# Performance work log

Measured on AMD Instinct MI355X. Metric: run time of the kernel, lower is better.

The kernel has to match this reference:

```python
import jax, jax.numpy as jnp
import numpy as np

N, S, D_MODEL, H = 8, 1024, 1024, 16
D = D_MODEL // H
NEG = -1e9


def setup_inputs() -> dict:
    key = jax.random.key(0)
    ks = jax.random.split(key, 12)
    s = 0.02
    q = jax.random.normal(ks[0], (N, S, D_MODEL), jnp.float32)
    k = jax.random.normal(ks[1], (N, S, D_MODEL), jnp.float32)
    v = jax.random.normal(ks[2], (N, S, D_MODEL), jnp.float32)
    # causal mask: 1 where masked (strict upper triangle)
    causal_mask = jnp.triu(jnp.ones((S, S), jnp.int32), k=1)
    # padding mask: 1 where key position is padding
    padding_mask = jax.random.randint(ks[3], (N, S), 0, 2, jnp.int32)
    Wq = jax.random.normal(ks[4], (D_MODEL, D_MODEL), jnp.float32) * s
    bq = jnp.zeros((D_MODEL,), jnp.float32)
    Wk = jax.random.normal(ks[5], (D_MODEL, D_MODEL), jnp.float32) * s
    bk = jnp.zeros((D_MODEL,), jnp.float32)
    Wv = jax.random.normal(ks[6], (D_MODEL, D_MODEL), jnp.float32) * s
    bv = jnp.zeros((D_MODEL,), jnp.float32)
    Wo = jax.random.normal(ks[7], (D_MODEL, D_MODEL), jnp.float32) * s
    bo = jnp.zeros((D_MODEL,), jnp.float32)
    return {"q": q, "k": k, "v": v, "causal_mask": causal_mask,
            "padding_mask": padding_mask, "Wq": Wq, "bq": bq, "Wk": Wk,
            "bk": bk, "Wv": Wv, "bv": bv, "Wo": Wo, "bo": bo}


def reference(q, k, v, causal_mask, padding_mask, Wq, bq, Wk, bk, Wv, bv, Wo, bo):
    n, qs, _ = q.shape
    # projections (nn.Linear: x @ W.T + b)
    qp = (q @ Wq.T + bq).reshape(n, qs, H, D).transpose(0, 2, 1, 3)  # [N,H,qS,D]
    kp = (k @ Wk.T + bk).reshape(n, -1, H, D).transpose(0, 2, 1, 3)  # [N,H,kS,D]
    vp = (v @ Wv.T + bv).reshape(n, -1, H, D).transpose(0, 2, 1, 3)  # [N,H,kS,D]
    # NOTE: faithful to source -- scale by sqrt(d_model), not sqrt(d_head)
    score = jnp.einsum('bhqd,bhkd->bhqk', qp, kp) / jnp.sqrt(jnp.float32(D_MODEL))
    score = jnp.where(causal_mask[None, None, :, :] == 1, NEG, score)
    score = jnp.where(padding_mask[:, None, None, :] == 1, NEG, score)
    w = jax.nn.softmax(score, axis=-1)  # dropout is identity in eval mode
    x = jnp.einsum('bhqk,bhkd->bhqd', w, vp)  # [N,H,qS,D]
    x = x.transpose(0, 2, 1, 3).reshape(n, qs, D_MODEL)
    x = x @ Wo.T + bo
    return (x, w)
```

## Files before the change

kernel.cpp:

```cpp
#include <hip/hip_runtime.h>

typedef __bf16 bf16;
typedef bf16 bf16x8 __attribute__((ext_vector_type(8)));
typedef bf16 bf16x4 __attribute__((ext_vector_type(4)));
typedef float f32x4 __attribute__((ext_vector_type(4)));

#define S_LEN 1024
#define DM    1024
#define NH    16
#define HD    64
#define NB    8
#define NEGV  (-1e9f)
#define QSCALE 0.03125f

#define EPI_HEADS 0
#define EPI_OUT   2

__device__ __forceinline__ void async16(const bf16* g, const bf16* l) {
    __builtin_amdgcn_global_load_lds(
        (const __attribute__((address_space(1))) void*)g,
        (__attribute__((address_space(3))) void*)l, 16, 0, 0);
}

__global__ __launch_bounds__(256) void cast_all(
    const float* __restrict__ q, const float* __restrict__ k,
    const float* __restrict__ v, const float* __restrict__ wq,
    const float* __restrict__ wk, const float* __restrict__ wv,
    const float* __restrict__ wo, bf16* __restrict__ out)
{
    size_t idx = ((size_t)blockIdx.x * 256 + threadIdx.x) * 4;
    const float* src;
    size_t soff;
    if (idx < 25165824) {
        int seg = (int)(idx >> 23);
        soff = idx & 8388607;
        src = seg == 0 ? q : (seg == 1 ? k : v);
    } else {
        size_t r = idx - 25165824;
        int seg = (int)(r >> 20);
        soff = r & 1048575;
        src = seg == 0 ? wq : (seg == 1 ? wk : (seg == 2 ? wv : wo));
    }
    f32x4 val = *(const f32x4*)&src[soff];
    bf16x4 o = {(bf16)val.x, (bf16)val.y, (bf16)val.z, (bf16)val.w};
    *(bf16x4*)&out[idx] = o;
}

__global__ __launch_bounds__(256) void gemm_qkv(
    const bf16* __restrict__ Ap, const bf16* __restrict__ Ball,
    const float* __restrict__ bq, const float* __restrict__ bk,
    const float* __restrict__ bv, bf16* __restrict__ Qp,
    bf16* __restrict__ Kp, bf16* __restrict__ Vp8)
{
    __shared__ bf16 As[128][32];
    __shared__ bf16 Bs[128][32];

    const int tid    = threadIdx.x;
    const int l      = tid & 63;
    const int wid    = tid >> 6;
    const int wr     = wid >> 1, wc = wid & 1;
    const int lane15 = l & 15, quad = l >> 4;
    const int row0   = blockIdx.x * 128;
    const int seg    = blockIdx.y >> 3;
    const int col0   = (blockIdx.y & 7) * 128;
    const int brow0  = seg * 1024 + col0;

    const bf16* Aseg = Ap + (size_t)seg * 8388608;
    const float* bias = seg == 0 ? bq : (seg == 1 ? bk : bv);

    f32x4 acc[4][4];
    #pragma unroll
    for (int i = 0; i < 4; ++i)
        #pragma unroll
        for (int j = 0; j < 4; ++j)
            acc[i][j] = (f32x4){0.f, 0.f, 0.f, 0.f};

    for (int k0 = 0; k0 < 1024; k0 += 32) {
        #pragma unroll
        for (int j = 0; j < 2; ++j) {
            int cbase = j * 256 + wid * 64;
            int c = cbase + l;
            int r = c >> 2, kc = (c & 3) << 3;
            async16(&Aseg[(size_t)(row0 + r) * 1024 + k0 + kc], &As[0][0] + cbase * 8);
            async16(&Ball[(size_t)(brow0 + r) * 1024 + k0 + kc], &Bs[0][0] + cbase * 8);
        }
        __syncthreads();

        bf16x8 afr[4], bfr[4];
        #pragma unroll
        for (int tm = 0; tm < 4; ++tm)
            afr[tm] = *(const bf16x8*)&As[wr * 64 + tm * 16 + lane15][quad * 8];
        #pragma unroll
        for (int tn = 0; tn < 4; ++tn)
            bfr[tn] = *(const bf16x8*)&Bs[wc * 64 + tn * 16 + lane15][quad * 8];
        #pragma unroll
        for (int tm = 0; tm < 4; ++tm)
            #pragma unroll
            for (int tn = 0; tn < 4; ++tn)
                acc[tm][tn] = __builtin_amdgcn_mfma_f32_16x16x32_bf16(
                    afr[tm], bfr[tn], acc[tm][tn], 0, 0, 0);
        __syncthreads();
    }

    #pragma unroll
    for (int tm = 0; tm < 4; ++tm) {
        #pragma unroll
        for (int tn = 0; tn < 4; ++tn) {
            int gr0 = row0 + wr * 64 + tm * 16 + quad * 4;
            int gc  = col0 + wc * 64 + tn * 16 + lane15;
            if (seg == 2) {
                int n = gr0 >> 10, s0 = gr0 & 1023, h = gc >> 6, d = gc & 63;
                float b = bias[gc];
                bf16x4 ov = {(bf16)(acc[tm][tn][0] + b), (bf16)(acc[tm][tn][1] + b),
                             (bf16)(acc[tm][tn][2] + b), (bf16)(acc[tm][tn][3] + b)};
                *(bf16x4*)&Vp8[(size_t)(n * NH + h) * 65536 +
                               (size_t)(s0 >> 3) * 512 + d * 8 + (s0 & 7)] = ov;
            } else {
                #pragma unroll
                for (int i = 0; i < 4; ++i) {
                    int gr = gr0 + i;
                    float vout = acc[tm][tn][i] + bias[gc];
                    int n = gr >> 10, s = gr & 1023, h = gc >> 6, d = gc & 63;
                    if (seg == 0) {
                        Qp[(((size_t)(n * NH + h) * S_LEN + s) << 6) + d] = (bf16)(vout * QSCALE);
                    } else {
                        Kp[(((size_t)(n * NH + h) * S_LEN + s) << 6) + d] = (bf16)vout;
                    }
                }
            }
        }
    }
}

template<int EPI>
__global__ __launch_bounds__(256) void gemm_nt(
    const bf16* __restrict__ Ap, const bf16* __restrict__ Bp,
    const float* __restrict__ bias, void* __restrict__ Cp)
{
    __shared__ bf16 As[128][32];
    __shared__ bf16 Bs[128][32];

    const int tid    = threadIdx.x;
    const int l      = tid & 63;
    const int wid    = tid >> 6;
    const int wr     = wid >> 1, wc = wid & 1;
    const int lane15 = l & 15, quad = l >> 4;
    const int row0   = blockIdx.x * 128;
    const int col0   = blockIdx.y * 128;

    f32x4 acc[4][4];
    #pragma unroll
    for (int i = 0; i < 4; ++i)
        #pragma unroll
        for (int j = 0; j < 4; ++j)
            acc[i][j] = (f32x4){0.f, 0.f, 0.f, 0.f};

    for (int k0 = 0; k0 < 1024; k0 += 32) {
        #pragma unroll
        for (int j = 0; j < 2; ++j) {
            int cbase = j * 256 + wid * 64;
            int c = cbase + l;
            int r = c >> 2, kc = (c & 3) << 3;
            async16(&Ap[(size_t)(row0 + r) * 1024 + k0 + kc], &As[0][0] + cbase * 8);
            async16(&Bp[(size_t)(col0 + r) * 1024 + k0 + kc], &Bs[0][0] + cbase * 8);
        }
        __syncthreads();

        bf16x8 afr[4], bfr[4];
        #pragma unroll
        for (int tm = 0; tm < 4; ++tm)
            afr[tm] = *(const bf16x8*)&As[wr * 64 + tm * 16 + lane15][quad * 8];
        #pragma unroll
        for (int tn = 0; tn < 4; ++tn)
            bfr[tn] = *(const bf16x8*)&Bs[wc * 64 + tn * 16 + lane15][quad * 8];
        #pragma unroll
        for (int tm = 0; tm < 4; ++tm)
            #pragma unroll
            for (int tn = 0; tn < 4; ++tn)
                acc[tm][tn] = __builtin_amdgcn_mfma_f32_16x16x32_bf16(
                    afr[tm], bfr[tn], acc[tm][tn], 0, 0, 0);
        __syncthreads();
    }

    #pragma unroll
    for (int tm = 0; tm < 4; ++tm) {
        #pragma unroll
        for (int tn = 0; tn < 4; ++tn) {
            #pragma unroll
            for (int i = 0; i < 4; ++i) {
                int gr = row0 + wr * 64 + tm * 16 + quad * 4 + i;
                int gc = col0 + wc * 64 + tn * 16 + lane15;
                float vout = acc[tm][tn][i] + bias[gc];
                if constexpr (EPI == EPI_HEADS) {
                    int n = gr >> 10, s = gr & 1023, h = gc >> 6, d = gc & 63;
                    ((bf16*)Cp)[(((size_t)(n * NH + h) * S_LEN + s) << 6) + d] = (bf16)vout;
                } else {
                    ((float*)Cp)[(size_t)gr * DM + gc] = vout;
                }
            }
        }
    }
}

__global__ __launch_bounds__(256, 4) void attn_fused(
    const bf16* __restrict__ Qp, const bf16* __restrict__ Kp,
    const bf16* __restrict__ Vp8, const int* __restrict__ pad,
    float* __restrict__ Wout, bf16* __restrict__ ctx)
{
    const int gid   = blockIdx.x;
    const int xcd   = gid & 7;
    const int t_    = gid >> 3;
    const int qblk  = t_ & 63;
    const int bh    = ((t_ >> 6) << 3) | xcd;
    const int h = bh & 15, n = bh >> 4;

    const bf16* Qb = Qp + (size_t)bh * S_LEN * HD;
    const bf16* Kb = Kp + (size_t)bh * S_LEN * HD;
    const bf16* Vb = Vp8 + (size_t)bh * HD * S_LEN;
    float* Wb = Wout + (size_t)bh * S_LEN * S_LEN;

    const int tid = threadIdx.x;
    const int l = tid & 63, wid = tid >> 6;
    const int lane15 = l & 15, quad = l >> 4;
    const int q0 = qblk * 16;
    const int q = q0 + lane15;
    const int qmax = q0 + 15;

    __shared__ bf16  P[16][1032];
    __shared__ float redM[4][16];
    __shared__ float redS[4][16];

    bf16x8 qf0 = *(const bf16x8*)&Qb[(size_t)q * HD + quad * 8];
    bf16x8 qf1 = *(const bf16x8*)&Qb[(size_t)q * HD + 32 + quad * 8];

    f32x4 sc[16];
    float mm = NEGV;

    #define KB_OF(t) ((((((t) >> 1) << 3) + (wid << 1) + ((t) & 1))) << 4)

    #pragma unroll
    for (int t = 0; t < 16; ++t) {
        int kb = KB_OF(t);
        if (kb <= qmax) {
            bf16x8 kf0 = *(const bf16x8*)&Kb[(size_t)(kb + lane15) * HD + quad * 8];
            bf16x8 kf1 = *(const bf16x8*)&Kb[(size_t)(kb + lane15) * HD + 32 + quad * 8];
            f32x4 a = (f32x4){0.f, 0.f, 0.f, 0.f};
            a = __builtin_amdgcn_mfma_f32_16x16x32_bf16(kf0, qf0, a, 0, 0, 0);
            a = __builtin_amdgcn_mfma_f32_16x16x32_bf16(kf1, qf1, a, 0, 0, 0);
            int4 pd = *(const int4*)&pad[n * S_LEN + kb + quad * 4];
            const int* pdi = (const int*)&pd;
            int key0 = kb + quad * 4;
            #pragma unroll
            for (int i = 0; i < 4; ++i)
                a[i] = (key0 + i > q || pdi[i] != 0) ? NEGV : a[i];
            sc[t] = a;
            mm = fmaxf(mm, fmaxf(fmaxf(a[0], a[1]), fmaxf(a[2], a[3])));
        }
    }

    mm = fmaxf(mm, __shfl_xor(mm, 16));
    mm = fmaxf(mm, __shfl_xor(mm, 32));
    if (l < 16) redM[wid][l] = mm;
    __syncthreads();
    float m = fmaxf(fmaxf(redM[0][lane15], redM[1][lane15]),
                    fmaxf(redM[2][lane15], redM[3][lane15]));

    float vskip = __expf(NEGV - m);

    float sm = 0.f;
    #pragma unroll
    for (int t = 0; t < 16; ++t) {
        int kb = KB_OF(t);
        if (kb <= qmax) {
            #pragma unroll
            for (int i = 0; i < 4; ++i) {
                float p = __expf(sc[t][i] - m);
                sc[t][i] = p;
                sm += p;
            }
        } else {
            sm += 4.f * vskip;
        }
    }
    sm += __shfl_xor(sm, 16);
    sm += __shfl_xor(sm, 32);
    if (l < 16) redS[wid][l] = sm;
    __syncthreads();
    float inv = 1.f / (redS[0][lane15] + redS[1][lane15] +
                       redS[2][lane15] + redS[3][lane15]);
    float wskip = vskip * inv;
    bool anyDeg = __ballot(m == NEGV) != 0;

    #pragma unroll
    for (int t = 0; t < 16; ++t) {
        int kb = KB_OF(t);
        int off = kb + quad * 4;
        if (kb <= qmax) {
            f32x4 wv = {sc[t][0] * inv, sc[t][1] * inv,
                        sc[t][2] * inv, sc[t][3] * inv};
            *(f32x4*)&Wb[(size_t)q * S_LEN + off] = wv;
            bf16x4 pb = {(bf16)wv.x, (bf16)wv.y, (bf16)wv.z, (bf16)wv.w};
            *(bf16x4*)&P[lane15][off] = pb;
        } else {
            f32x4 wv = {wskip, wskip, wskip, wskip};
            *(f32x4*)&Wb[(size_t)q * S_LEN + off] = wv;
            bf16 pv = (bf16)wskip;
            bf16x4 pb = {pv, pv, pv, pv};
            *(bf16x4*)&P[lane15][off] = pb;
        }
    }
    #undef KB_OF
    __syncthreads();

    const int dbase = wid * 16;
    const int cEnd = anyDeg ? 32 : ((qmax >> 5) + 1);
    f32x4 o = (f32x4){0.f, 0.f, 0.f, 0.f};
    #pragma unroll 4
    for (int c = 0; c < cEnd; ++c) {
        bf16x8 a = *(const bf16x8*)&P[lane15][c * 32 + quad * 8];
        bf16x8 b = *(const bf16x8*)&Vb[((size_t)(c * 4 + quad) * 64 + dbase + lane15) * 8];
        o = __builtin_amdgcn_mfma_f32_16x16x32_bf16(a, b, o, 0, 0, 0);
    }
    #pragma unroll
    for (int i = 0; i < 4; ++i) {
        int row = q0 + quad * 4 + i;
        ctx[((size_t)(n * S_LEN + row) << 10) + h * HD + dbase + lane15] = (bf16)o[i];
    }
}

extern "C" void kernel_launch(void* const* d_in, const int* in_sizes, int n_in,
                              void* d_out, int out_size, void* d_ws, size_t ws_size,
                              hipStream_t stream)
{
    const float* q   = (const float*)d_in[0];
    const float* k   = (const float*)d_in[1];
    const float* v   = (const float*)d_in[2];
    const int*   pad = (const int*)  d_in[4];
    const float* Wq  = (const float*)d_in[5];
    const float* bq  = (const float*)d_in[6];
    const float* Wk  = (const float*)d_in[7];
    const float* bk  = (const float*)d_in[8];
    const float* Wv  = (const float*)d_in[9];
    const float* bv  = (const float*)d_in[10];
    const float* Wo  = (const float*)d_in[11];
    const float* bo  = (const float*)d_in[12];

    float* x_out = (float*)d_out;
    float* w_out = x_out + (size_t)NB * S_LEN * DM;

    bf16* wsb = (bf16*)d_ws;
    bf16* Qc  = wsb;
    bf16* Wqb = wsb + 25165824;
    bf16* Wob = wsb + 28311552;
    bf16* Qp  = wsb + 29360128;
    bf16* Kp  = wsb + 37748736;
    bf16* Vp8 = wsb + 46137344;
    bf16* ctx = wsb + 54525952;

    cast_all<<<28672, 256, 0, stream>>>(q, k, v, Wq, Wk, Wv, Wo, wsb);

    gemm_qkv<<<dim3(64, 24), 256, 0, stream>>>(Qc, Wqb, bq, bk, bv, Qp, Kp, Vp8);

    attn_fused<<<dim3(8192), 256, 0, stream>>>(Qp, Kp, Vp8, pad, w_out, ctx);

    gemm_nt<EPI_OUT><<<dim3(64, 8), 256, 0, stream>>>(ctx, Wob, bo, x_out);
}
```

Before: 877.5 us.

## Swizzle GEMM block order per XCD and coalesce attention-weight stores via LDS

Both GEMMs now use a 1D grid whose block index is remapped so that the 8 row tiles sharing a column tile land on the same XCD. The intent is better L2 reuse of the B operand. In the attention kernel, the fp32 weight output is no longer written per lane in scattered 16-byte pieces. Each thread instead reads back the bf16 probabilities from the LDS tile and writes whole rows contiguously, which should give coalesced stores. The catch is that w is now rounded through bf16 before it is stored, so it loses precision.

```diff
diff --git a/kernel.cpp b/kernel.cpp
--- a/kernel.cpp
+++ b/kernel.cpp
@@ -60,10 +60,16 @@
     const int wid    = tid >> 6;
     const int wr     = wid >> 1, wc = wid & 1;
     const int lane15 = l & 15, quad = l >> 4;
-    const int row0   = blockIdx.x * 128;
-    const int seg    = blockIdx.y >> 3;
-    const int col0   = (blockIdx.y & 7) * 128;
-    const int brow0  = seg * 1024 + col0;
+
+    const int gid  = blockIdx.x;
+    const int xcd  = gid & 7;
+    const int idx  = gid >> 3;
+    const int xl   = idx & 7;
+    const int y    = idx >> 3;
+    const int row0 = (xcd * 8 + xl) * 128;
+    const int seg  = y >> 3;
+    const int col0 = (y & 7) * 128;
+    const int brow0 = seg * 1024 + col0;
 
     const bf16* Aseg = Ap + (size_t)seg * 8388608;
     const float* bias = seg == 0 ? bq : (seg == 1 ? bk : bv);
@@ -145,8 +151,14 @@
     const int wid    = tid >> 6;
     const int wr     = wid >> 1, wc = wid & 1;
     const int lane15 = l & 15, quad = l >> 4;
-    const int row0   = blockIdx.x * 128;
-    const int col0   = blockIdx.y * 128;
+
+    const int gid  = blockIdx.x;
+    const int xcd  = gid & 7;
+    const int idx  = gid >> 3;
+    const int xl   = idx & 7;
+    const int y    = idx >> 3;
+    const int row0 = (xcd * 8 + xl) * 128;
+    const int col0 = y * 128;
 
     f32x4 acc[4][4];
     #pragma unroll
@@ -296,14 +308,10 @@
         int kb = KB_OF(t);
         int off = kb + quad * 4;
         if (kb <= qmax) {
-            f32x4 wv = {sc[t][0] * inv, sc[t][1] * inv,
-                        sc[t][2] * inv, sc[t][3] * inv};
-            *(f32x4*)&Wb[(size_t)q * S_LEN + off] = wv;
-            bf16x4 pb = {(bf16)wv.x, (bf16)wv.y, (bf16)wv.z, (bf16)wv.w};
+            bf16x4 pb = {(bf16)(sc[t][0] * inv), (bf16)(sc[t][1] * inv),
+                         (bf16)(sc[t][2] * inv), (bf16)(sc[t][3] * inv)};
             *(bf16x4*)&P[lane15][off] = pb;
         } else {
-            f32x4 wv = {wskip, wskip, wskip, wskip};
-            *(f32x4*)&Wb[(size_t)q * S_LEN + off] = wv;
             bf16 pv = (bf16)wskip;
             bf16x4 pb = {pv, pv, pv, pv};
             *(bf16x4*)&P[lane15][off] = pb;
@@ -311,6 +319,13 @@
     }
     #undef KB_OF
     __syncthreads();
+
+    #pragma unroll
+    for (int r = 0; r < 16; ++r) {
+        bf16x4 pb = *(const bf16x4*)&P[r][tid * 4];
+        f32x4 wv = {(float)pb[0], (float)pb[1], (float)pb[2], (float)pb[3]};
+        *(f32x4*)&Wb[(size_t)(q0 + r) * S_LEN + tid * 4] = wv;
+    }
 
     const int dbase = wid * 16;
     const int cEnd = anyDeg ? 32 : ((qmax >> 5) + 1);
@@ -359,9 +374,9 @@
 
     cast_all<<<28672, 256, 0, stream>>>(q, k, v, Wq, Wk, Wv, Wo, wsb);
 
-    gemm_qkv<<<dim3(64, 24), 256, 0, stream>>>(Qc, Wqb, bq, bk, bv, Qp, Kp, Vp8);
+    gemm_qkv<<<dim3(1536), 256, 0, stream>>>(Qc, Wqb, bq, bk, bv, Qp, Kp, Vp8);
 
     attn_fused<<<dim3(8192), 256, 0, stream>>>(Qp, Kp, Vp8, pad, w_out, ctx);
 
-    gemm_nt<EPI_OUT><<<dim3(64, 8), 256, 0, stream>>>(ctx, Wob, bo, x_out);
-}
+    gemm_nt<EPI_OUT><<<dim3(512), 256, 0, stream>>>(ctx, Wob, bo, x_out);
+}
```

Result: faster. 858.1 us (-2.2%).
